# Kernel tuning notes

Hardware: AMD Instinct MI355X
Metric: run time of the kernel (lower is better)

The kernel has to match this reference:

```python
import jax, jax.numpy as jnp
import numpy as np

# Constants from the module's __init__ (LIFNodes / RUMNodes / Connection args)
DT = 1.0
TAU = 10.0            # LIF membrane time constant
TC_TRACE = 20.0       # spike-trace time constant (bindsnet default)
REST, RESET, THRESH = -70.0, -65.0, -55.0
ALPHA, BETA = 0.95, 0.8     # RUM hidden leak / threshold-adaptation decay
H_THRESH = 1.0              # hidden firing threshold
NU1_PRE, NU1_POST = 0.001, 0.01    # PostPre STDP rates (input->hidden)
NU2 = 0.0001                        # MSTDP learning rate (hidden->output)
WMIN, WMAX = 0.0, 1.0
REWARD = 1.0
A_PLUS, A_MINUS = 1.0, -1.0         # MSTDP trace amplitudes (bindsnet defaults)
TC_PM = 20.0                        # MSTDP p_plus/p_minus time constant
INPUT_GAIN = 20.0   # scales U[0,1) rates into the LIF operating range (rest->thresh gap = 15 mV)

IN_D, HID_D, OUT_D = 544, 1024, 2048


def setup_inputs() -> dict:
    key = jax.random.key(0)
    k1, k2, k3 = jax.random.split(key, 3)
    x = jax.random.uniform(k1, (IN_D,), dtype=jnp.float32)            # rate-coded input
    w1 = jax.random.uniform(k2, (IN_D, HID_D), dtype=jnp.float32)     # in [wmin, wmax]
    w2 = jax.random.uniform(k3, (HID_D, OUT_D), dtype=jnp.float32)
    return {"x": x, "w1": w1, "w2": w2, "num_timesteps": 500}


def _simulate(x, w1, w2, T):
    decay_v = jnp.float32(np.exp(-DT / TAU))
    decay_tr = jnp.float32(np.exp(-DT / TC_TRACE))
    decay_pm = jnp.float32(np.exp(-DT / TC_PM))
    rates = x * INPUT_GAIN  # constant input current each timestep (rate coding)

    carry = (
        jnp.full((IN_D,), REST, jnp.float32),   # v_in
        jnp.zeros((HID_D,), jnp.float32),        # v_hid
        jnp.full((OUT_D,), REST, jnp.float32),   # v_out
        jnp.zeros((IN_D,), jnp.float32),         # tr_in  (pre trace, PostPre)
        jnp.zeros((HID_D,), jnp.float32),        # tr_hid (post trace, PostPre)
        jnp.zeros((HID_D,), jnp.float32),        # b_hid  (RUM threshold adaptation)
        jnp.zeros((HID_D,), jnp.float32),        # p_plus  (MSTDP pre trace)
        jnp.zeros((OUT_D,), jnp.float32),        # p_minus (MSTDP post trace)
        w1, w2,
    )

    def step(c, _):
        v_in, v_hid, v_out, tr_in, tr_hid, b_hid, p_plus, p_minus, w1c, w2c = c
        # --- input LIF: decay toward rest, integrate rates, spike, reset ---
        v_in = decay_v * (v_in - REST) + REST + rates
        s_in = (v_in >= THRESH).astype(jnp.float32)
        v_in = jnp.where(s_in > 0, RESET, v_in)
        tr_in = jnp.where(s_in > 0, 1.0, tr_in * decay_tr)
        # --- hidden RUM: leaky integration (alpha) + adaptive threshold (beta) ---
        i_hid = s_in @ w1c                                  # [HID]
        v_hid = ALPHA * v_hid + i_hid
        s_hid = (v_hid >= H_THRESH + b_hid).astype(jnp.float32)
        v_hid = jnp.where(s_hid > 0, 0.0, v_hid)
        b_hid = BETA * b_hid + s_hid
        tr_hid_new = jnp.where(s_hid > 0, 1.0, tr_hid * decay_tr)
        # --- output LIF ---
        i_out = s_hid @ w2c                                 # [OUT]
        v_out = decay_v * (v_out - REST) + REST + i_out
        s_out = (v_out >= THRESH).astype(jnp.float32)
        v_out = jnp.where(s_out > 0, RESET, v_out)
        # --- PostPre STDP on w1: potentiate on post spike, depress on pre spike ---
        w1c = jnp.clip(
            w1c + NU1_POST * jnp.outer(tr_in, s_hid) - NU1_PRE * jnp.outer(s_in, tr_hid_new),
            WMIN, WMAX)
        # --- MSTDP on w2: reward-modulated eligibility ---
        p_plus = decay_pm * p_plus + A_PLUS * s_hid
        p_minus = decay_pm * p_minus + A_MINUS * s_out
        elig = jnp.outer(p_plus, s_out) + jnp.outer(s_hid, p_minus)  # [HID, OUT]
        w2c = w2c + NU2 * REWARD * DT * elig
        new_c = (v_in, v_hid, v_out, tr_in, tr_hid_new, b_hid, p_plus, p_minus, w1c, w2c)
        return new_c, s_out

    _, spikes = jax.lax.scan(step, carry, None, length=T)
    return spikes  # [T, OUT_D] float32 spike raster (== stacked monitor recording)


def reference(x, w1, w2, num_timesteps):
    return _simulate(x, w1, w2, num_timesteps)
```

## Files before the change

kernel.cpp:

```cpp
#include <hip/hip_runtime.h>
#include <stdint.h>


#define DECAY_V  0.90483741803595952f
#define DECAY_TR 0.95122942450071403f
#define REST_F   (-70.0f)
#define RESET_F  (-65.0f)
#define THRESH_F (-55.0f)
#define ALPHA_F  (0.95f)
#define BETA_F   (0.8f)
#define NU1_PRE_F  (0.001f)
#define NU1_POST_F (0.01f)
#define NU2_F      (0.0001f)
#define GAIN_F     (20.0f)
#define LOG2D    (-0.072134752044448170f)

static constexpr int IN_D  = 544;
static constexpr int HID_D = 1024;
static constexpr int OUT_D = 2048;
static constexpr int TMAX  = 512;

#define DP1  0.95122942450071403f
#define DP2  0.90483741803595957f
#define DP4  0.81873075307798186f
#define DP8  0.67032004603563930f
#define DP16 0.44932896411722159f
#define DP32 0.20189651799465541f

__device__ __forceinline__ float rdlane(float x, int l) {
    return __builtin_bit_cast(float,
        __builtin_amdgcn_readlane(__builtin_bit_cast(int, x), l));
}

template <int CTRL>
__device__ __forceinline__ float dpp_add(float x) {
    int y = __builtin_amdgcn_update_dpp(0, __builtin_bit_cast(int, x),
                                        CTRL, 0xF, 0xF, true);
    return x + __builtin_bit_cast(float, y);
}

__device__ __forceinline__ float wave_sum64(float x) {
    x = dpp_add<0xB1>(x);
    x = dpp_add<0x4E>(x);
    x = dpp_add<0x114>(x);
    x = dpp_add<0x118>(x);
    x = dpp_add<0x142>(x);
    x = dpp_add<0x143>(x);
    return rdlane(x, 63);
}

__global__ __launch_bounds__(256, 2)
void hidden_kernel(const float* __restrict__ x, const float* __restrict__ w1,
                   const int* __restrict__ Tp, float* __restrict__ Sf)
{
    const int T = Tp[0];
    const int tid = threadIdx.x, lane = tid & 63, wv = tid >> 6;
    const int cp = wv >> 1;
    const int h  = wv & 1;
    const int col = blockIdx.x * 2 + cp;
    const float c0 = REST_F * (1.0f - DECAY_V);
    __shared__ float part[2][4];

    float w[5], vi[5], tr[5], cadd[5];
    #pragma unroll
    for (int k = 0; k < 5; ++k) {
        const int o = 64 * k + lane;
        const int i = 272 * h + o;
        const bool ok = (o < 272);
        w[k]    = ok ? w1[(size_t)i * HID_D + col] : 0.f;
        cadd[k] = c0 + (ok ? x[i] * GAIN_F : 0.f);
        vi[k]   = REST_F;
        tr[k]   = 0.f;
    }
    float v_h = 0.f, b_h = 0.f, tr_h = 0.f;

    for (int t = 0; t < T; ++t) {
        float acc = 0.f, s[5];
        #pragma unroll
        for (int k = 0; k < 5; ++k) {
            const float vv = fmaf(DECAY_V, vi[k], cadd[k]);
            const bool sp = (vv >= THRESH_F);
            vi[k] = sp ? RESET_F : vv;
            s[k]  = sp ? 1.f : 0.f;
            tr[k] = fmaxf(tr[k] * DECAY_TR, s[k]);
            acc   = fmaf(s[k], w[k], acc);
        }
        const float p = wave_sum64(acc);
        const int par = t & 1;
        if (lane == 0) part[par][wv] = p;
        __syncthreads();
        const float tot = p + part[par][wv ^ 1];
        const float vh2 = fmaf(ALPHA_F, v_h, tot);
        const bool hp = (vh2 >= 1.0f + b_h);
        const float sh = hp ? 1.f : 0.f;
        v_h  = hp ? 0.f : vh2;
        b_h  = fmaf(BETA_F, b_h, sh);
        tr_h = hp ? 1.f : tr_h * DECAY_TR;
        const float apot = hp ? NU1_POST_F : 0.f;
        const float adep = NU1_PRE_F * tr_h;
        #pragma unroll
        for (int k = 0; k < 5; ++k) {
            const float a  = fmaf(apot, tr[k], w[k]);
            const float nw = fmaf(-adep, s[k], a);
            w[k] = __builtin_amdgcn_fmed3f(nw, 0.f, 1.f);
        }
        if (h == 0 && lane == 0) Sf[(size_t)t * HID_D + col] = sh;
    }
}

__global__ void pack_kernel(float* __restrict__ Sf, const int* __restrict__ Tp,
                            unsigned long long* __restrict__ Sb)
{
    const int T = Tp[0];
    const int t = blockIdx.x;
    const int lane = threadIdx.x & 63, wv = threadIdx.x >> 6;
    if (t >= T) {
        ((float4*)(Sf + (size_t)t * HID_D))[threadIdx.x] = make_float4(0.f, 0.f, 0.f, 0.f);
        return;
    }
    #pragma unroll
    for (int q = 0; q < 4; ++q) {
        const int word = wv * 4 + q;
        const float s = Sf[(size_t)t * HID_D + word * 64 + lane];
        const unsigned long long m = __ballot(s > 0.5f);
        if (lane == 0) Sb[(size_t)t * 16 + word] = m;
    }
}

__global__ void gram_kernel(const unsigned long long* __restrict__ Sb,
                            const int* __restrict__ Tp, float* __restrict__ G)
{
    const int T = Tp[0];
    if ((int)blockIdx.x > (int)blockIdx.y) return;
    const int tid = threadIdx.x;
    __shared__ unsigned long long tR[16][17], uR[16][17];
    {
        const int r = tid >> 4, w = tid & 15;
        const int trow = blockIdx.y * 16 + r, urow = blockIdx.x * 16 + r;
        tR[r][w] = (trow < T) ? Sb[(size_t)trow * 16 + w] : 0ULL;
        uR[r][w] = (urow < T) ? Sb[(size_t)urow * 16 + w] : 0ULL;
    }
    __syncthreads();
    const int tx = tid & 15, ty = tid >> 4;
    const int t = blockIdx.y * 16 + ty, u = blockIdx.x * 16 + tx;
    if (t < T && u < t) {
        int s = 0;
        #pragma unroll
        for (int w = 0; w < 16; ++w) s += __popcll(tR[ty][w] & uR[tx][w]);
        G[(size_t)t * TMAX + u] = (float)s;
    }
}

__global__ __launch_bounds__(256)
void mt_kernel(const float* __restrict__ G, const int* __restrict__ Tp,
               float* __restrict__ MT)
{
    const int T = Tp[0];
    const int lane = threadIdx.x & 63;
    const int t = blockIdx.x * 4 + (threadIdx.x >> 6);
    if (t >= T) return;
    const float* Gr = G + (size_t)t * TMAX;
    const float dl1  = exp2f((float)(lane + 1) * LOG2D);
    const float d64l = exp2f((float)(64 - lane) * LOG2D);

    float g[8], kk[8];
    #pragma unroll
    for (int c = 0; c < 8; ++c) {
        const int tau = 64 * c + lane;
        g[c] = (tau < t) ? Gr[tau] : 0.f;
    }
    float kc = 0.f;
    #pragma unroll
    for (int c = 7; c >= 0; --c) {
        float k = g[c], u;
        u = __shfl_down(k, 1, 64);  if (lane < 63) k = fmaf(DP1, u, k);
        u = __shfl_down(k, 2, 64);  if (lane < 62) k = fmaf(DP2, u, k);
        u = __shfl_down(k, 4, 64);  if (lane < 60) k = fmaf(DP4, u, k);
        u = __shfl_down(k, 8, 64);  if (lane < 56) k = fmaf(DP8, u, k);
        u = __shfl_down(k, 16, 64); if (lane < 48) k = fmaf(DP16, u, k);
        u = __shfl_down(k, 32, 64); if (lane < 32) k = fmaf(DP32, u, k);
        k = fmaf(d64l, kc, k);
        kk[c] = k;
        kc = rdlane(k, 0);
    }
    float hc = 0.f;
    #pragma unroll
    for (int c = 0; c < 8; ++c) {
        float h = g[c], u;
        u = __shfl_up(h, 1, 64);  if (lane >= 1)  h = fmaf(DP1, u, h);
        u = __shfl_up(h, 2, 64);  if (lane >= 2)  h = fmaf(DP2, u, h);
        u = __shfl_up(h, 4, 64);  if (lane >= 4)  h = fmaf(DP4, u, h);
        u = __shfl_up(h, 8, 64);  if (lane >= 8)  h = fmaf(DP8, u, h);
        u = __shfl_up(h, 16, 64); if (lane >= 16) h = fmaf(DP16, u, h);
        u = __shfl_up(h, 32, 64); if (lane >= 32) h = fmaf(DP32, u, h);
        h = fmaf(dl1, hc, h);
        const int tau = 64 * c + lane;
        if (tau < t) MT[(size_t)tau * TMAX + t] = NU2_F * (h - kk[c]);
        hc = rdlane(h, 63);
    }
}

__global__ __launch_bounds__(256)
void gemm_kernel(const float* __restrict__ Sf, const float* __restrict__ w2,
                 float* __restrict__ AT, int klen)
{
    const int j0 = blockIdx.x * 128;
    const int t0 = blockIdx.y * 64;
    const int kbase = blockIdx.z * 512;
    float* ATp = AT + (size_t)blockIdx.z * OUT_D * TMAX;
    __shared__ float Ss[16][68];
    __shared__ float Ws[16][192];
    const int tid = threadIdx.x;
    const int sr = tid >> 2, sq = tid & 3;
    const int wq2 = tid & 31, wr2 = tid >> 5;
    const int wcol = (wq2 >> 1) * 12 + (wq2 & 1) * 4;
    const int tj = tid & 15, tt = tid >> 4;
    const int tjc = tj * 12;

    float acc[4][8];
    #pragma unroll
    for (int a = 0; a < 4; ++a)
        #pragma unroll
        for (int b = 0; b < 8; ++b) acc[a][b] = 0.f;

    for (int k0 = 0; k0 < klen; k0 += 16) {
        const float4 sv = *(const float4*)&Sf[(size_t)(t0 + sr) * HID_D + kbase + k0 + sq * 4];
        const float4 wa = *(const float4*)&w2[(size_t)(kbase + k0 + wr2) * OUT_D + j0 + wq2 * 4];
        const float4 wb = *(const float4*)&w2[(size_t)(kbase + k0 + wr2 + 8) * OUT_D + j0 + wq2 * 4];
        __syncthreads();
        Ss[sq * 4 + 0][sr] = sv.x;
        Ss[sq * 4 + 1][sr] = sv.y;
        Ss[sq * 4 + 2][sr] = sv.z;
        Ss[sq * 4 + 3][sr] = sv.w;
        *(float4*)&Ws[wr2][wcol] = wa;
        *(float4*)&Ws[wr2 + 8][wcol] = wb;
        __syncthreads();
        #pragma unroll
        for (int kk = 0; kk < 16; ++kk) {
            const float4 a4 = *(const float4*)&Ss[kk][tt * 4];
            const float4 b0 = *(const float4*)&Ws[kk][tjc];
            const float4 b1 = *(const float4*)&Ws[kk][tjc + 4];
            const float aa[4] = {a4.x, a4.y, a4.z, a4.w};
            const float bb[8] = {b0.x, b0.y, b0.z, b0.w, b1.x, b1.y, b1.z, b1.w};
            #pragma unroll
            for (int ti = 0; ti < 4; ++ti)
                #pragma unroll
                for (int jj = 0; jj < 8; ++jj)
                    acc[ti][jj] = fmaf(aa[ti], bb[jj], acc[ti][jj]);
        }
    }
    #pragma unroll
    for (int jj = 0; jj < 8; ++jj)
        *(float4*)&AT[(size_t)blockIdx.z * OUT_D * TMAX +
                      (size_t)(j0 + tj * 8 + jj) * TMAX + t0 + tt * 4] =
            make_float4(acc[0][jj], acc[1][jj], acc[2][jj], acc[3][jj]);
    (void)ATp;
}

template <int C>
__device__ __forceinline__ void out_chunk(
    const float* __restrict__ AT, const float* __restrict__ MT,
    float (&hsA)[8], float (&hsB)[8], float& vA, float& vB,
    float* __restrict__ out, int j, int lane, int T, int nparts,
    float* __restrict__ LD, float2* __restrict__ so2)
{
    const int rem = T - 64 * C;
    const int mtv = (rem < 64) ? rem : 64;
    float avA = AT[(size_t)j * TMAX + 64 * C + lane];
    float avB = AT[(size_t)(j + 1) * TMAX + 64 * C + lane];
    if (nparts == 2) {
        avA += AT[(size_t)(OUT_D + j) * TMAX + 64 * C + lane];
        avB += AT[(size_t)(OUT_D + j + 1) * TMAX + 64 * C + lane];
    }
    const float* ldb = LD + (C & 1) * 4096;
    float accA = hsA[C], accB = hsB[C];
    float mv0 = ldb[lane];
    float mv1 = (mtv > 1) ? ldb[64 + lane] : 0.f;
    for (int tt = 0; tt < mtv; ++tt) {
        const float mv = mv0;
        mv0 = mv1;
        if (tt + 2 < mtv) mv1 = ldb[(tt + 2) * 64 + lane];
        const float ivA = rdlane(avA + accA, tt);
        const float ivB = rdlane(avB + accB, tt);
        const float vdA = fmaf(DECAY_V, vA, REST_F * (1.0f - DECAY_V)) + ivA;
        const float vdB = fmaf(DECAY_V, vB, REST_F * (1.0f - DECAY_V)) + ivB;
        const bool spA = (vdA >= THRESH_F);
        const bool spB = (vdB >= THRESH_F);
        const float soA = spA ? 1.f : 0.f;
        const float soB = spB ? 1.f : 0.f;
        vA = spA ? RESET_F : vdA;
        vB = spB ? RESET_F : vdB;
        if (lane == 0)
            *(float2*)&out[(size_t)(64 * C + tt) * OUT_D + j] = make_float2(soA, soB);
        if (lane == tt) so2[tt] = make_float2(soA, soB);
        accA = fmaf(soA, mv, accA);
        accB = fmaf(soB, mv, accB);
    }
    if (C + 1 < 8 && 64 * (C + 1) < T) {
        {
            float* dst = LD + ((C + 1) & 1) * 4096;
            const float* src = MT + (size_t)(64 * (C + 1)) * TMAX + 64 * (C + 1) + lane;
            #pragma unroll 16
            for (int r = 0; r < 64; ++r) {
                const float v = src[(size_t)r * TMAX];
                dst[r * 64 + lane] = (r < lane) ? v : 0.f;
            }
        }
        for (int tt = 0; tt < mtv; ++tt) {
            const float2 s = so2[tt];
            const float* Mrow = MT + (size_t)(64 * C + tt) * TMAX + lane;
            #pragma unroll
            for (int K = C + 1; K < 8; ++K) {
                const float mval = Mrow[64 * K];
                hsA[K] = fmaf(s.x, mval, hsA[K]);
                hsB[K] = fmaf(s.y, mval, hsB[K]);
            }
        }
    }
}

__global__ __launch_bounds__(64, 2)
void out_kernel(const float* __restrict__ AT, const float* __restrict__ MT,
                const int* __restrict__ Tp, float* __restrict__ out, int nparts)
{
    const int T = Tp[0];
    const int lane = threadIdx.x;
    const int j = blockIdx.x * 2;
    __shared__ float LD[2 * 4096];
    __shared__ float2 so2[64];

    float hsA[8], hsB[8];
    #pragma unroll
    for (int k = 0; k < 8; ++k) { hsA[k] = 0.f; hsB[k] = 0.f; }
    float vA = REST_F, vB = REST_F;

    {
        const float* src = MT + lane;
        #pragma unroll 16
        for (int r = 0; r < 64; ++r) {
            const float v = src[(size_t)r * TMAX];
            LD[r * 64 + lane] = (r < lane) ? v : 0.f;
        }
    }
    out_chunk<0>(AT, MT, hsA, hsB, vA, vB, out, j, lane, T, nparts, LD, so2);
    if (T >  64) out_chunk<1>(AT, MT, hsA, hsB, vA, vB, out, j, lane, T, nparts, LD, so2);
    if (T > 128) out_chunk<2>(AT, MT, hsA, hsB, vA, vB, out, j, lane, T, nparts, LD, so2);
    if (T > 192) out_chunk<3>(AT, MT, hsA, hsB, vA, vB, out, j, lane, T, nparts, LD, so2);
    if (T > 256) out_chunk<4>(AT, MT, hsA, hsB, vA, vB, out, j, lane, T, nparts, LD, so2);
    if (T > 320) out_chunk<5>(AT, MT, hsA, hsB, vA, vB, out, j, lane, T, nparts, LD, so2);
    if (T > 384) out_chunk<6>(AT, MT, hsA, hsB, vA, vB, out, j, lane, T, nparts, LD, so2);
    if (T > 448) out_chunk<7>(AT, MT, hsA, hsB, vA, vB, out, j, lane, T, nparts, LD, so2);
}

extern "C" void kernel_launch(void* const* d_in, const int* in_sizes, int n_in,
                              void* d_out, int out_size, void* d_ws, size_t ws_size,
                              hipStream_t stream) {
    const float* x  = (const float*)d_in[0];
    const float* w1 = (const float*)d_in[1];
    const float* w2 = (const float*)d_in[2];
    const int*   Tp = (const int*)d_in[3];
    float* out = (float*)d_out;
    char* ws = (char*)d_ws;
    unsigned long long* Sb = (unsigned long long*)(ws);
    float* G  = (float*)(ws + 65536);
    float* MT = (float*)(ws + 65536 + 1048576);
    float* Sf = (float*)(ws + 65536 + 2 * 1048576);
    float* AT = (float*)(ws + 65536 + 4 * 1048576);
    const size_t need2 = 65536 + 4 * 1048576 + 2 * 4194304;
    const int nparts = (ws_size >= need2) ? 2 : 1;
    const int klen = (nparts == 2) ? 512 : 1024;

    hipLaunchKernelGGL(hidden_kernel, dim3(HID_D / 2), dim3(256), 0, stream, x, w1, Tp, Sf);
    hipLaunchKernelGGL(pack_kernel,   dim3(TMAX), dim3(256), 0, stream, Sf, Tp, Sb);
    hipLaunchKernelGGL(gram_kernel,   dim3(32, 32), dim3(256), 0, stream, Sb, Tp, G);
    hipLaunchKernelGGL(mt_kernel,     dim3(128), dim3(256), 0, stream, G, Tp, MT);
    hipLaunchKernelGGL(gemm_kernel,   dim3(16, 8, nparts), dim3(256), 0, stream,
                       Sf, w2, AT, klen);
    hipLaunchKernelGGL(out_kernel,    dim3(OUT_D / 2), dim3(64), 0, stream, AT, MT, Tp, out, nparts);
}
```

Before: 321.6 us.

## Fuse gram and gemm launches, widen out kernel to 4 columns, unroll hidden loop

Merges the popcount Gram kernel and the spike-by-w2 GEMM into one launch that picks its role from the block index, removing one kernel launch and letting both phases share the GPU. The GEMM K-split can now use 4 partial parts when the workspace allows, which gives more blocks. The output LIF recurrence now handles 4 output columns per 64-lane block instead of 2, halving block count and amortising the LD tile loads and the serial loop. The hidden loop is also unrolled by two with fixed parity. In exchange the out kernel uses more registers and has fewer blocks to spread across the GPU.

```diff
diff --git a/kernel.cpp b/kernel.cpp
--- a/kernel.cpp
+++ b/kernel.cpp
@@ -73,8 +73,9 @@
         tr[k]   = 0.f;
     }
     float v_h = 0.f, b_h = 0.f, tr_h = 0.f;
-
-    for (int t = 0; t < T; ++t) {
+    const bool writer = (h == 0 && lane == 0);
+
+    auto step = [&](int t, int par) {
         float acc = 0.f, s[5];
         #pragma unroll
         for (int k = 0; k < 5; ++k) {
@@ -86,7 +87,6 @@
             acc   = fmaf(s[k], w[k], acc);
         }
         const float p = wave_sum64(acc);
-        const int par = t & 1;
         if (lane == 0) part[par][wv] = p;
         __syncthreads();
         const float tot = p + part[par][wv ^ 1];
@@ -104,8 +104,15 @@
             const float nw = fmaf(-adep, s[k], a);
             w[k] = __builtin_amdgcn_fmed3f(nw, 0.f, 1.f);
         }
-        if (h == 0 && lane == 0) Sf[(size_t)t * HID_D + col] = sh;
-    }
+        if (writer) Sf[(size_t)t * HID_D + col] = sh;
+    };
+
+    int t = 0;
+    for (; t + 1 < T; t += 2) {
+        step(t, 0);
+        step(t + 1, 1);
+    }
+    if (t < T) step(t, 0);
 }
 
 __global__ void pack_kernel(float* __restrict__ Sf, const int* __restrict__ Tp,
@@ -127,27 +134,86 @@
     }
 }
 
-__global__ void gram_kernel(const unsigned long long* __restrict__ Sb,
-                            const int* __restrict__ Tp, float* __restrict__ G)
-{
-    const int T = Tp[0];
-    if ((int)blockIdx.x > (int)blockIdx.y) return;
-    const int tid = threadIdx.x;
-    __shared__ unsigned long long tR[16][17], uR[16][17];
-    {
-        const int r = tid >> 4, w = tid & 15;
-        const int trow = blockIdx.y * 16 + r, urow = blockIdx.x * 16 + r;
-        tR[r][w] = (trow < T) ? Sb[(size_t)trow * 16 + w] : 0ULL;
-        uR[r][w] = (urow < T) ? Sb[(size_t)urow * 16 + w] : 0ULL;
-    }
-    __syncthreads();
-    const int tx = tid & 15, ty = tid >> 4;
-    const int t = blockIdx.y * 16 + ty, u = blockIdx.x * 16 + tx;
-    if (t < T && u < t) {
-        int s = 0;
-        #pragma unroll
-        for (int w = 0; w < 16; ++w) s += __popcll(tR[ty][w] & uR[tx][w]);
-        G[(size_t)t * TMAX + u] = (float)s;
+__global__ __launch_bounds__(256)
+void gramgemm_kernel(const unsigned long long* __restrict__ Sb,
+                     const int* __restrict__ Tp, float* __restrict__ G,
+                     const float* __restrict__ Sf, const float* __restrict__ w2,
+                     float* __restrict__ AT, int klen)
+{
+    __shared__ __align__(16) char smem[16640];
+    const int b = blockIdx.x, tid = threadIdx.x;
+    if (b < 1024) {
+        const int by = b >> 5, bx = b & 31;
+        if (bx > by) return;
+        const int T = Tp[0];
+        typedef unsigned long long u64;
+        u64 (*tR)[17] = (u64(*)[17])(smem);
+        u64 (*uR)[17] = (u64(*)[17])(smem + 2176);
+        {
+            const int r = tid >> 4, w0 = tid & 15;
+            const int trow = by * 16 + r, urow = bx * 16 + r;
+            tR[r][w0] = (trow < T) ? Sb[(size_t)trow * 16 + w0] : 0ULL;
+            uR[r][w0] = (urow < T) ? Sb[(size_t)urow * 16 + w0] : 0ULL;
+        }
+        __syncthreads();
+        const int tx = tid & 15, ty = tid >> 4;
+        const int t = by * 16 + ty, u = bx * 16 + tx;
+        if (t < T && u < t) {
+            int s = 0;
+            #pragma unroll
+            for (int w0 = 0; w0 < 16; ++w0) s += __popcll(tR[ty][w0] & uR[tx][w0]);
+            G[(size_t)t * TMAX + u] = (float)s;
+        }
+    } else {
+        const int g = b - 1024;
+        const int z = g >> 7, r = g & 127;
+        const int j0 = (r & 15) * 128, t0 = (r >> 4) * 64;
+        const int kbase = z * klen;
+        float (*Ss)[68]  = (float(*)[68])(smem);
+        float (*Ws)[192] = (float(*)[192])(smem + 4352);
+        const int sr = tid >> 2, sq = tid & 3;
+        const int wq2 = tid & 31, wr2 = tid >> 5;
+        const int wcol = (wq2 >> 1) * 12 + (wq2 & 1) * 4;
+        const int tj = tid & 15, tt = tid >> 4;
+        const int tjc = tj * 12;
+
+        float acc[4][8];
+        #pragma unroll
+        for (int a = 0; a < 4; ++a)
+            #pragma unroll
+            for (int bb = 0; bb < 8; ++bb) acc[a][bb] = 0.f;
+
+        for (int k0 = 0; k0 < klen; k0 += 16) {
+            const float4 sv = *(const float4*)&Sf[(size_t)(t0 + sr) * HID_D + kbase + k0 + sq * 4];
+            const float4 wa = *(const float4*)&w2[(size_t)(kbase + k0 + wr2) * OUT_D + j0 + wq2 * 4];
+            const float4 wb = *(const float4*)&w2[(size_t)(kbase + k0 + wr2 + 8) * OUT_D + j0 + wq2 * 4];
+            __syncthreads();
+            Ss[sq * 4 + 0][sr] = sv.x;
+            Ss[sq * 4 + 1][sr] = sv.y;
+            Ss[sq * 4 + 2][sr] = sv.z;
+            Ss[sq * 4 + 3][sr] = sv.w;
+            *(float4*)&Ws[wr2][wcol] = wa;
+            *(float4*)&Ws[wr2 + 8][wcol] = wb;
+            __syncthreads();
+            #pragma unroll
+            for (int kk = 0; kk < 16; ++kk) {
+                const float4 a4 = *(const float4*)&Ss[kk][tt * 4];
+                const float4 b0 = *(const float4*)&Ws[kk][tjc];
+                const float4 b1 = *(const float4*)&Ws[kk][tjc + 4];
+                const float aa[4] = {a4.x, a4.y, a4.z, a4.w};
+                const float bbv[8] = {b0.x, b0.y, b0.z, b0.w, b1.x, b1.y, b1.z, b1.w};
+                #pragma unroll
+                for (int ti = 0; ti < 4; ++ti)
+                    #pragma unroll
+                    for (int jj = 0; jj < 8; ++jj)
+                        acc[ti][jj] = fmaf(aa[ti], bbv[jj], acc[ti][jj]);
+            }
+        }
+        #pragma unroll
+        for (int jj = 0; jj < 8; ++jj)
+            *(float4*)&AT[(size_t)z * OUT_D * TMAX +
+                          (size_t)(j0 + tj * 8 + jj) * TMAX + t0 + tt * 4] =
+                make_float4(acc[0][jj], acc[1][jj], acc[2][jj], acc[3][jj]);
     }
 }
 
@@ -200,120 +266,69 @@
     }
 }
 
-__global__ __launch_bounds__(256)
-void gemm_kernel(const float* __restrict__ Sf, const float* __restrict__ w2,
-                 float* __restrict__ AT, int klen)
-{
-    const int j0 = blockIdx.x * 128;
-    const int t0 = blockIdx.y * 64;
-    const int kbase = blockIdx.z * 512;
-    float* ATp = AT + (size_t)blockIdx.z * OUT_D * TMAX;
-    __shared__ float Ss[16][68];
-    __shared__ float Ws[16][192];
-    const int tid = threadIdx.x;
-    const int sr = tid >> 2, sq = tid & 3;
-    const int wq2 = tid & 31, wr2 = tid >> 5;
-    const int wcol = (wq2 >> 1) * 12 + (wq2 & 1) * 4;
-    const int tj = tid & 15, tt = tid >> 4;
-    const int tjc = tj * 12;
-
-    float acc[4][8];
-    #pragma unroll
-    for (int a = 0; a < 4; ++a)
-        #pragma unroll
-        for (int b = 0; b < 8; ++b) acc[a][b] = 0.f;
-
-    for (int k0 = 0; k0 < klen; k0 += 16) {
-        const float4 sv = *(const float4*)&Sf[(size_t)(t0 + sr) * HID_D + kbase + k0 + sq * 4];
-        const float4 wa = *(const float4*)&w2[(size_t)(kbase + k0 + wr2) * OUT_D + j0 + wq2 * 4];
-        const float4 wb = *(const float4*)&w2[(size_t)(kbase + k0 + wr2 + 8) * OUT_D + j0 + wq2 * 4];
-        __syncthreads();
-        Ss[sq * 4 + 0][sr] = sv.x;
-        Ss[sq * 4 + 1][sr] = sv.y;
-        Ss[sq * 4 + 2][sr] = sv.z;
-        Ss[sq * 4 + 3][sr] = sv.w;
-        *(float4*)&Ws[wr2][wcol] = wa;
-        *(float4*)&Ws[wr2 + 8][wcol] = wb;
-        __syncthreads();
-        #pragma unroll
-        for (int kk = 0; kk < 16; ++kk) {
-            const float4 a4 = *(const float4*)&Ss[kk][tt * 4];
-            const float4 b0 = *(const float4*)&Ws[kk][tjc];
-            const float4 b1 = *(const float4*)&Ws[kk][tjc + 4];
-            const float aa[4] = {a4.x, a4.y, a4.z, a4.w};
-            const float bb[8] = {b0.x, b0.y, b0.z, b0.w, b1.x, b1.y, b1.z, b1.w};
-            #pragma unroll
-            for (int ti = 0; ti < 4; ++ti)
-                #pragma unroll
-                for (int jj = 0; jj < 8; ++jj)
-                    acc[ti][jj] = fmaf(aa[ti], bb[jj], acc[ti][jj]);
-        }
-    }
-    #pragma unroll
-    for (int jj = 0; jj < 8; ++jj)
-        *(float4*)&AT[(size_t)blockIdx.z * OUT_D * TMAX +
-                      (size_t)(j0 + tj * 8 + jj) * TMAX + t0 + tt * 4] =
-            make_float4(acc[0][jj], acc[1][jj], acc[2][jj], acc[3][jj]);
-    (void)ATp;
-}
-
 template <int C>
 __device__ __forceinline__ void out_chunk(
     const float* __restrict__ AT, const float* __restrict__ MT,
-    float (&hsA)[8], float (&hsB)[8], float& vA, float& vB,
+    float (&hs)[4][8], float (&v)[4],
     float* __restrict__ out, int j, int lane, int T, int nparts,
-    float* __restrict__ LD, float2* __restrict__ so2)
+    float* __restrict__ LD, float4* __restrict__ so4)
 {
     const int rem = T - 64 * C;
     const int mtv = (rem < 64) ? rem : 64;
-    float avA = AT[(size_t)j * TMAX + 64 * C + lane];
-    float avB = AT[(size_t)(j + 1) * TMAX + 64 * C + lane];
-    if (nparts == 2) {
-        avA += AT[(size_t)(OUT_D + j) * TMAX + 64 * C + lane];
-        avB += AT[(size_t)(OUT_D + j + 1) * TMAX + 64 * C + lane];
+    float av[4];
+    #pragma unroll
+    for (int q = 0; q < 4; ++q) {
+        float a = AT[(size_t)(j + q) * TMAX + 64 * C + lane];
+        for (int p = 1; p < nparts; ++p)
+            a += AT[(size_t)p * OUT_D * TMAX + (size_t)(j + q) * TMAX + 64 * C + lane];
+        av[q] = a;
     }
     const float* ldb = LD + (C & 1) * 4096;
-    float accA = hsA[C], accB = hsB[C];
+    float acc[4];
+    #pragma unroll
+    for (int q = 0; q < 4; ++q) acc[q] = hs[q][C];
     float mv0 = ldb[lane];
     float mv1 = (mtv > 1) ? ldb[64 + lane] : 0.f;
     for (int tt = 0; tt < mtv; ++tt) {
         const float mv = mv0;
         mv0 = mv1;
         if (tt + 2 < mtv) mv1 = ldb[(tt + 2) * 64 + lane];
-        const float ivA = rdlane(avA + accA, tt);
-        const float ivB = rdlane(avB + accB, tt);
-        const float vdA = fmaf(DECAY_V, vA, REST_F * (1.0f - DECAY_V)) + ivA;
-        const float vdB = fmaf(DECAY_V, vB, REST_F * (1.0f - DECAY_V)) + ivB;
-        const bool spA = (vdA >= THRESH_F);
-        const bool spB = (vdB >= THRESH_F);
-        const float soA = spA ? 1.f : 0.f;
-        const float soB = spB ? 1.f : 0.f;
-        vA = spA ? RESET_F : vdA;
-        vB = spB ? RESET_F : vdB;
+        float so[4];
+        #pragma unroll
+        for (int q = 0; q < 4; ++q) {
+            const float iv = rdlane(av[q] + acc[q], tt);
+            const float vd = fmaf(DECAY_V, v[q], REST_F * (1.0f - DECAY_V)) + iv;
+            const bool sp = (vd >= THRESH_F);
+            so[q] = sp ? 1.f : 0.f;
+            v[q]  = sp ? RESET_F : vd;
+        }
         if (lane == 0)
-            *(float2*)&out[(size_t)(64 * C + tt) * OUT_D + j] = make_float2(soA, soB);
-        if (lane == tt) so2[tt] = make_float2(soA, soB);
-        accA = fmaf(soA, mv, accA);
-        accB = fmaf(soB, mv, accB);
+            *(float4*)&out[(size_t)(64 * C + tt) * OUT_D + j] =
+                make_float4(so[0], so[1], so[2], so[3]);
+        if (lane == tt) so4[tt] = make_float4(so[0], so[1], so[2], so[3]);
+        #pragma unroll
+        for (int q = 0; q < 4; ++q) acc[q] = fmaf(so[q], mv, acc[q]);
     }
     if (C + 1 < 8 && 64 * (C + 1) < T) {
         {
             float* dst = LD + ((C + 1) & 1) * 4096;
             const float* src = MT + (size_t)(64 * (C + 1)) * TMAX + 64 * (C + 1) + lane;
             #pragma unroll 16
-            for (int r = 0; r < 64; ++r) {
-                const float v = src[(size_t)r * TMAX];
-                dst[r * 64 + lane] = (r < lane) ? v : 0.f;
+            for (int rr = 0; rr < 64; ++rr) {
+                const float vv = src[(size_t)rr * TMAX];
+                dst[rr * 64 + lane] = (rr < lane) ? vv : 0.f;
             }
         }
         for (int tt = 0; tt < mtv; ++tt) {
-            const float2 s = so2[tt];
+            const float4 s = so4[tt];
             const float* Mrow = MT + (size_t)(64 * C + tt) * TMAX + lane;
             #pragma unroll
             for (int K = C + 1; K < 8; ++K) {
                 const float mval = Mrow[64 * K];
-                hsA[K] = fmaf(s.x, mval, hsA[K]);
-                hsB[K] = fmaf(s.y, mval, hsB[K]);
+                hs[0][K] = fmaf(s.x, mval, hs[0][K]);
+                hs[1][K] = fmaf(s.y, mval, hs[1][K]);
+                hs[2][K] = fmaf(s.z, mval, hs[2][K]);
+                hs[3][K] = fmaf(s.w, mval, hs[3][K]);
             }
         }
     }
@@ -325,31 +340,33 @@
 {
     const int T = Tp[0];
     const int lane = threadIdx.x;
-    const int j = blockIdx.x * 2;
+    const int j = blockIdx.x * 4;
     __shared__ float LD[2 * 4096];
-    __shared__ float2 so2[64];
-
-    float hsA[8], hsB[8];
-    #pragma unroll
-    for (int k = 0; k < 8; ++k) { hsA[k] = 0.f; hsB[k] = 0.f; }
-    float vA = REST_F, vB = REST_F;
+    __shared__ float4 so4[64];
+
+    float hs[4][8];
+    #pragma unroll
+    for (int q = 0; q < 4; ++q)
+        #pragma unroll
+        for (int k = 0; k < 8; ++k) hs[q][k] = 0.f;
+    float v[4] = {REST_F, REST_F, REST_F, REST_F};
 
     {
         const float* src = MT + lane;
         #pragma unroll 16
-        for (int r = 0; r < 64; ++r) {
-            const float v = src[(size_t)r * TMAX];
-            LD[r * 64 + lane] = (r < lane) ? v : 0.f;
-        }
-    }
-    out_chunk<0>(AT, MT, hsA, hsB, vA, vB, out, j, lane, T, nparts, LD, so2);
-    if (T >  64) out_chunk<1>(AT, MT, hsA, hsB, vA, vB, out, j, lane, T, nparts, LD, so2);
-    if (T > 128) out_chunk<2>(AT, MT, hsA, hsB, vA, vB, out, j, lane, T, nparts, LD, so2);
-    if (T > 192) out_chunk<3>(AT, MT, hsA, hsB, vA, vB, out, j, lane, T, nparts, LD, so2);
-    if (T > 256) out_chunk<4>(AT, MT, hsA, hsB, vA, vB, out, j, lane, T, nparts, LD, so2);
-    if (T > 320) out_chunk<5>(AT, MT, hsA, hsB, vA, vB, out, j, lane, T, nparts, LD, so2);
-    if (T > 384) out_chunk<6>(AT, MT, hsA, hsB, vA, vB, out, j, lane, T, nparts, LD, so2);
-    if (T > 448) out_chunk<7>(AT, MT, hsA, hsB, vA, vB, out, j, lane, T, nparts, LD, so2);
+        for (int rr = 0; rr < 64; ++rr) {
+            const float vv = src[(size_t)rr * TMAX];
+            LD[rr * 64 + lane] = (rr < lane) ? vv : 0.f;
+        }
+    }
+    out_chunk<0>(AT, MT, hs, v, out, j, lane, T, nparts, LD, so4);
+    if (T >  64) out_chunk<1>(AT, MT, hs, v, out, j, lane, T, nparts, LD, so4);
+    if (T > 128) out_chunk<2>(AT, MT, hs, v, out, j, lane, T, nparts, LD, so4);
+    if (T > 192) out_chunk<3>(AT, MT, hs, v, out, j, lane, T, nparts, LD, so4);
+    if (T > 256) out_chunk<4>(AT, MT, hs, v, out, j, lane, T, nparts, LD, so4);
+    if (T > 320) out_chunk<5>(AT, MT, hs, v, out, j, lane, T, nparts, LD, so4);
+    if (T > 384) out_chunk<6>(AT, MT, hs, v, out, j, lane, T, nparts, LD, so4);
+    if (T > 448) out_chunk<7>(AT, MT, hs, v, out, j, lane, T, nparts, LD, so4);
 }
 
 extern "C" void kernel_launch(void* const* d_in, const int* in_sizes, int n_in,
@@ -366,15 +383,15 @@
     float* MT = (float*)(ws + 65536 + 1048576);
     float* Sf = (float*)(ws + 65536 + 2 * 1048576);
     float* AT = (float*)(ws + 65536 + 4 * 1048576);
-    const size_t need2 = 65536 + 4 * 1048576 + 2 * 4194304;
-    const int nparts = (ws_size >= need2) ? 2 : 1;
-    const int klen = (nparts == 2) ? 512 : 1024;
+    const size_t base  = 65536 + 4 * 1048576;
+    const int nparts = (ws_size >= base + 4 * 4194304) ? 4
+                     : (ws_size >= base + 2 * 4194304) ? 2 : 1;
+    const int klen = 1024 / nparts;
 
     hipLaunchKernelGGL(hidden_kernel, dim3(HID_D / 2), dim3(256), 0, stream, x, w1, Tp, Sf);
     hipLaunchKernelGGL(pack_kernel,   dim3(TMAX), dim3(256), 0, stream, Sf, Tp, Sb);
-    hipLaunchKernelGGL(gram_kernel,   dim3(32, 32), dim3(256), 0, stream, Sb, Tp, G);
+    hipLaunchKernelGGL(gramgemm_kernel, dim3(1024 + 128 * nparts), dim3(256), 0, stream,
+                       Sb, Tp, G, Sf, w2, AT, klen);
     hipLaunchKernelGGL(mt_kernel,     dim3(128), dim3(256), 0, stream, G, Tp, MT);
-    hipLaunchKernelGGL(gemm_kernel,   dim3(16, 8, nparts), dim3(256), 0, stream,
-                       Sf, w2, AT, klen);
-    hipLaunchKernelGGL(out_kernel,    dim3(OUT_D / 2), dim3(64), 0, stream, AT, MT, Tp, out, nparts);
-}
+    hipLaunchKernelGGL(out_kernel,    dim3(OUT_D / 4), dim3(64), 0, stream, AT, MT, Tp, out, nparts);
+}
```

Result: slower. 343.2 us (+6.7%).
